# Kernel tuning notes

Measured on AMD Instinct MI355X. Metric: run time of the kernel, lower is better.

Reference implementation:

```python
import jax, jax.numpy as jnp
import numpy as np

K = 3
STRIDE = 1
PAD = 1


def conv2d(x, w, b):
    # standard NCHW conv, stride 1, pad 1
    out = jax.lax.conv_general_dilated(
        x, w, (STRIDE, STRIDE), [(PAD, PAD), (PAD, PAD)],
        dimension_numbers=("NCHW", "OIHW", "NCHW"))
    return out + b[None, :, None, None]


def deform_conv2d(x, offset, mask, weight):
    # torchvision.ops.deform_conv2d semantics (offset_groups=1):
    # offset: [B, 2*K*K, Ho, Wo] laid out as (k, (y, x)) per kernel tap k (row-major)
    # mask:   [B, K*K, Ho, Wo]
    B, C, H, W = x.shape
    KK = K * K
    Ho, Wo = offset.shape[2:]
    off = offset.reshape(B, KK, 2, Ho, Wo)

    # base sampling positions: p = out*stride - pad + kernel_tap + offset
    tap_y = jnp.repeat(jnp.arange(K, dtype=x.dtype), K)  # [KK]
    tap_x = jnp.tile(jnp.arange(K, dtype=x.dtype), K)    # [KK]
    grid_y = jnp.arange(Ho, dtype=x.dtype) * STRIDE - PAD
    grid_x = jnp.arange(Wo, dtype=x.dtype) * STRIDE - PAD
    py = grid_y[None, None, :, None] + tap_y[None, :, None, None] + off[:, :, 0]  # [B,KK,Ho,Wo]
    px = grid_x[None, None, None, :] + tap_x[None, :, None, None] + off[:, :, 1]

    y0 = jnp.floor(py)
    x0 = jnp.floor(px)
    wy1 = py - y0  # fractional parts
    wx1 = px - x0

    xf = x.reshape(B, C, H * W)

    def gather(yi, xi):
        # zero-padding semantics: out-of-bounds corners contribute 0
        valid = (yi >= 0) & (yi <= H - 1) & (xi >= 0) & (xi <= W - 1)
        idx = (jnp.clip(yi, 0, H - 1) * W + jnp.clip(xi, 0, W - 1)).astype(jnp.int32)
        v = jnp.take_along_axis(xf, idx.reshape(B, 1, KK * Ho * Wo), axis=2)
        v = v.reshape(B, C, KK, Ho, Wo)
        return v * valid[:, None].astype(x.dtype)

    e = lambda a: a[:, None]  # [B,KK,Ho,Wo] -> [B,1,KK,Ho,Wo]
    sampled = (gather(y0, x0) * e((1 - wy1) * (1 - wx1))
               + gather(y0, x0 + 1) * e((1 - wy1) * wx1)
               + gather(y0 + 1, x0) * e(wy1 * (1 - wx1))
               + gather(y0 + 1, x0 + 1) * e(wy1 * wx1))
    sampled = sampled * mask[:, None]  # modulated, [B,C,KK,Ho,Wo]

    Cout = weight.shape[0]
    out = jnp.einsum("bckhw,ock->bohw", sampled, weight.reshape(Cout, C, KK))
    return out


def setup_inputs() -> dict:
    key = jax.random.key(0)
    ks = jax.random.split(key, 5)
    B, Cin, Cout, H, W = 4, 128, 256, 64, 64
    x = jax.random.normal(ks[0], (B, Cin, H, W), jnp.float32)
    # offset/modulator convs are zero-init in the module; use small random weights
    # so the deformable sampling path is actually exercised
    offset_w = jax.random.normal(ks[1], (2 * K * K, Cin, K, K), jnp.float32) * 0.02
    offset_b = jax.random.normal(ks[2], (2 * K * K,), jnp.float32) * 0.1
    mod_w = jax.random.normal(ks[3], (K * K, Cin, K, K), jnp.float32) * 0.02
    mod_b = jnp.zeros((K * K,), jnp.float32)
    weight = jax.random.normal(ks[4], (Cout, Cin, K, K), jnp.float32) * (1.0 / np.sqrt(Cin * K * K))
    return {"x": x, "offset_w": offset_w, "offset_b": offset_b,
            "mod_w": mod_w, "mod_b": mod_b, "weight": weight}


def reference(x, offset_w, offset_b, mod_w, mod_b, weight):
    H, W = x.shape[2], x.shape[3]
    max_offset = max(H, W) / 4.0
    offset = jnp.clip(conv2d(x, offset_w, offset_b), -max_offset, max_offset)
    mask = 2.0 * jax.nn.sigmoid(conv2d(x, mod_w, mod_b))
    return deform_conv2d(x, offset, mask, weight)
```

## Files before the change

kernel.cpp:

```cpp
#include <hip/hip_runtime.h>
#include <math.h>

#define CIN   128
#define COUT  256
#define HH    64
#define WW    64
#define BB    4
#define KK    9
#define CK    (CIN*KK)

typedef unsigned short u16;
typedef unsigned int   u32;
using f32x4  = __attribute__((ext_vector_type(4))) float;
using s16x8  = __attribute__((ext_vector_type(8))) short;

__device__ __forceinline__ u16 f2bf(float f) {
    union { float f; u32 u; } v; v.f = f;
    u32 u = v.u;
    u += 0x7FFFu + ((u >> 16) & 1u);
    return (u16)(u >> 16);
}
__device__ __forceinline__ float bfel(s16x8 v, int j) {
    union { u32 u; float f; } c; c.u = ((u32)(u16)v[j]) << 16; return c.f;
}
__device__ __forceinline__ u32 asu(float f) {
    union { float f; u32 u; } v; v.f = f; return v.u;
}

__global__ __launch_bounds__(256)
void prep_all(const float* __restrict__ x, const float* __restrict__ w,
              const float* __restrict__ ow, const float* __restrict__ mw,
              u16* __restrict__ xt, u16* __restrict__ wfrag,
              u16* __restrict__ wofsf) {
    __shared__ u16 T[64][130];
    int blk = blockIdx.x;
    int tid = threadIdx.x;

    if (blk < 256) {
        int b = blk >> 6, y = blk & 63;
        int lane = tid & 63, cw = tid >> 6;
        for (int c = cw; c < 128; c += 4)
            T[lane][c] = f2bf(x[((b * 128 + c) * 64 + y) * 64 + lane]);
        __syncthreads();
        int c = tid & 127;
        for (int p = tid >> 7; p < 64; p += 2)
            xt[((b * 64 + y) * 64 + p) * 128 + c] = T[p][c];
    } else if (blk < 256 + 1152) {
        int i = (blk - 256) * 256 + tid;
        int j    = i & 7;
        int lane = (i >> 3) & 63;
        int ks4  = (i >> 9) & 3;
        int t    = (i >> 11) & 1;
        int wv   = (i >> 12) & 7;
        int tap  = i >> 15;
        int co = (wv * 2 + t) * 16 + (lane & 15);
        int k  = tap * 128 + ks4 * 32 + (lane >> 4) * 8 + j;
        int c  = k & 127;
        wfrag[i] = f2bf(w[co * CK + c * 9 + tap]);
    } else {
        int i = (blk - 1408) * 256 + tid;
        if (i < 9 * 4096) {
            int j    = i & 7;
            int lane = (i >> 3) & 63;
            int ks4  = (i >> 9) & 3;
            int t    = (i >> 11) & 1;
            int tap  = i >> 12;
            int co = t * 16 + (lane & 15);
            int k  = tap * 128 + ks4 * 32 + (lane >> 4) * 8 + j;
            int c  = k & 127;
            float v = 0.f;
            if (co < 18)      v = ow[co * CK + c * 9 + tap];
            else if (co < 27) v = mw[(co - 18) * CK + c * 9 + tap];
            wofsf[i] = f2bf(v);
        }
    }
}

__global__ __launch_bounds__(512, 4)
void dcn_fused(const u16* __restrict__ xt, const u16* __restrict__ wofsf,
               const float* __restrict__ ob, const float* __restrict__ mb,
               const u16* __restrict__ wfrag, float* __restrict__ out) {
    int blkid = blockIdx.x;
    int xcd = blkid & 7, idx = blkid >> 3;
    int b   = xcd >> 1;
    int ho  = ((xcd & 1) << 5) + (idx >> 1);
    int wo0 = (idx & 1) << 5;
    int tid = threadIdx.x;

    __shared__ __align__(16) u16 Sm[4][32][136];
    __shared__ float s_om[27][32];
    __shared__ int   s_idx[32][KK][4];
    __shared__ float s_wgt[32][KK][4];

    int wv   = tid >> 6, lane = tid & 63;
    int quad = lane >> 4, l16 = lane & 15;
    int gpx  = wv * 4 + (lane >> 4);
    int oct  = lane & 15;

    const u16* xtb = xt + (size_t)b * 4096 * 128;
    const s16x8 vzero = {0,0,0,0,0,0,0,0};

    int pa_ph = wv & 1;
    f32x4 aco[2];
    aco[0] = (f32x4)(0.f); aco[1] = (f32x4)(0.f);

    s16x8 sA[2][2];
    auto pa_gather = [&](int tap, int sp, int ti) {
        int kx = tap % 3;
        int y  = ho - 1 + tap / 3;
        bool yok = (unsigned)y < HH;
        int col = wo0 + gpx + kx - 1;
        bool ok = yok && ((unsigned)col < WW);
        int yc = yok ? y : 0;
        int cc = ((unsigned)col < WW) ? col : 0;
        s16x8 v = *(const s16x8*)(xtb + (size_t)(yc * 64 + cc) * 128 + oct * 8);
        sA[sp][ti] = ok ? v : vzero;
    };

    auto pa_mfma_tap = [&](int tap, int slot) {
        const u16* wc = wofsf + tap * 4096 + lane * 8;
#pragma unroll
        for (int ks4 = 0; ks4 < 4; ++ks4) {
            s16x8 bfrag = *(const s16x8*)(&Sm[slot][pa_ph * 16 + l16][ks4 * 32 + quad * 8]);
#pragma unroll
            for (int t = 0; t < 2; ++t) {
                s16x8 afrag = *(const s16x8*)(wc + (t * 4 + ks4) * 512);
                aco[t] = __builtin_amdgcn_mfma_f32_16x16x32_bf16(afrag, bfrag, aco[t], 0, 0, 0);
            }
        }
    };

    pa_gather(0, 0, 0);
    pa_gather(1, 0, 1);
#pragma unroll
    for (int p = 0; p < 4; ++p) {
        int sp = p & 1;
        *(s16x8*)(&Sm[2 * sp    ][gpx][oct * 8]) = sA[sp][0];
        *(s16x8*)(&Sm[2 * sp + 1][gpx][oct * 8]) = sA[sp][1];
        __syncthreads();
        if (p < 3) { pa_gather(2 * p + 2, sp ^ 1, 0); pa_gather(2 * p + 3, sp ^ 1, 1); }
        else       { pa_gather(8,         sp ^ 1, 0); }
        if (wv < 2) {
            pa_mfma_tap(2 * p,     2 * sp);
            pa_mfma_tap(2 * p + 1, 2 * sp + 1);
        }
    }
    *(s16x8*)(&Sm[0][gpx][oct * 8]) = sA[0][0];
    __syncthreads();
    if (wv < 2) pa_mfma_tap(8, 0);

    if (wv < 2) {
#pragma unroll
        for (int t = 0; t < 2; ++t) {
#pragma unroll
            for (int r = 0; r < 4; ++r) {
                int co = t * 16 + quad * 4 + r;
                if (co < 27) {
                    float v = aco[t][r];
                    if (co < 18) {
                        v += ob[co];
                        v = fminf(fmaxf(v, -16.f), 16.f);
                    } else {
                        v += mb[co - 18];
                        v = 2.f / (1.f + expf(-v));
                    }
                    s_om[co][pa_ph * 16 + l16] = v;
                }
            }
        }
    }
    __syncthreads();

    if (tid < 32 * KK) {
        int p = tid / KK, k = tid - (tid / KK) * KK;
        int wo = wo0 + p;
        float offy = s_om[2 * k][p];
        float offx = s_om[2 * k + 1][p];
        float mval = s_om[18 + k][p];

        float py = (float)(ho - 1 + k / 3) + offy;
        float px = (float)(wo - 1 + k % 3) + offx;
        float y0f = floorf(py), x0f = floorf(px);
        float wy1 = py - y0f,  wx1 = px - x0f;
        float wy0 = 1.f - wy1, wx0 = 1.f - wx1;
        int iy0 = (int)y0f, ix0 = (int)x0f;
        int iy1 = iy0 + 1,  ix1 = ix0 + 1;
        bool vy0 = (iy0 >= 0) && (iy0 < HH);
        bool vy1 = (iy1 >= 0) && (iy1 < HH);
        bool vx0 = (ix0 >= 0) && (ix0 < WW);
        bool vx1 = (ix1 >= 0) && (ix1 < WW);
        int cy0 = min(max(iy0, 0), HH - 1), cy1 = min(max(iy1, 0), HH - 1);
        int cx0 = min(max(ix0, 0), WW - 1), cx1 = min(max(ix1, 0), WW - 1);
        s_idx[p][k][0] = (cy0 * WW + cx0) * 128;
        s_idx[p][k][1] = (cy0 * WW + cx1) * 128;
        s_idx[p][k][2] = (cy1 * WW + cx0) * 128;
        s_idx[p][k][3] = (cy1 * WW + cx1) * 128;
        s_wgt[p][k][0] = (vy0 && vx0) ? mval * wy0 * wx0 : 0.f;
        s_wgt[p][k][1] = (vy0 && vx1) ? mval * wy0 * wx1 : 0.f;
        s_wgt[p][k][2] = (vy1 && vx0) ? mval * wy1 * wx0 : 0.f;
        s_wgt[p][k][3] = (vy1 && vx1) ? mval * wy1 * wx1 : 0.f;
    }
    __syncthreads();

    f32x4 acc[2][2];
#pragma unroll
    for (int t = 0; t < 2; ++t) { acc[t][0] = (f32x4)(0.f); acc[t][1] = (f32x4)(0.f); }

    s16x8 crs[2][2][4];
    float gs[2][2][4];
    auto gatherB = [&](int tap, int sp, int ti) {
        int i0 = s_idx[gpx][tap][0], i1 = s_idx[gpx][tap][1];
        int i2 = s_idx[gpx][tap][2], i3 = s_idx[gpx][tap][3];
        gs[sp][ti][0] = s_wgt[gpx][tap][0]; gs[sp][ti][1] = s_wgt[gpx][tap][1];
        gs[sp][ti][2] = s_wgt[gpx][tap][2]; gs[sp][ti][3] = s_wgt[gpx][tap][3];
        int co8 = oct * 8;
        crs[sp][ti][0] = *(const s16x8*)(xtb + i0 + co8);
        crs[sp][ti][1] = *(const s16x8*)(xtb + i1 + co8);
        crs[sp][ti][2] = *(const s16x8*)(xtb + i2 + co8);
        crs[sp][ti][3] = *(const s16x8*)(xtb + i3 + co8);
    };

    auto blend_store = [&](int sp, int ti, int slot) {
        float g0 = gs[sp][ti][0], g1 = gs[sp][ti][1];
        float g2 = gs[sp][ti][2], g3 = gs[sp][ti][3];
        float o[8];
#pragma unroll
        for (int j = 0; j < 8; ++j)
            o[j] = g0 * bfel(crs[sp][ti][0], j) + g1 * bfel(crs[sp][ti][1], j)
                 + g2 * bfel(crs[sp][ti][2], j) + g3 * bfel(crs[sp][ti][3], j);
        uint4 pkv;
        pkv.x = (asu(o[1]) & 0xFFFF0000u) | (asu(o[0]) >> 16);
        pkv.y = (asu(o[3]) & 0xFFFF0000u) | (asu(o[2]) >> 16);
        pkv.z = (asu(o[5]) & 0xFFFF0000u) | (asu(o[4]) >> 16);
        pkv.w = (asu(o[7]) & 0xFFFF0000u) | (asu(o[6]) >> 16);
        *(uint4*)(&Sm[slot][gpx][oct * 8]) = pkv;
    };

    auto pb_mfma_tap = [&](int tap, int slot) {
        const u16* wc = wfrag + (tap * 8 + wv) * 4096 + lane * 8;
        s16x8 af[8];
#pragma unroll
        for (int t = 0; t < 2; ++t)
#pragma unroll
            for (int ks4 = 0; ks4 < 4; ++ks4)
                af[t * 4 + ks4] = *(const s16x8*)(wc + (t * 4 + ks4) * 512);
#pragma unroll
        for (int ks4 = 0; ks4 < 4; ++ks4) {
            s16x8 bf0 = *(const s16x8*)(&Sm[slot][l16][ks4 * 32 + quad * 8]);
            s16x8 bf1 = *(const s16x8*)(&Sm[slot][16 + l16][ks4 * 32 + quad * 8]);
#pragma unroll
            for (int t = 0; t < 2; ++t) {
                acc[t][0] = __builtin_amdgcn_mfma_f32_16x16x32_bf16(af[t * 4 + ks4], bf0, acc[t][0], 0, 0, 0);
                acc[t][1] = __builtin_amdgcn_mfma_f32_16x16x32_bf16(af[t * 4 + ks4], bf1, acc[t][1], 0, 0, 0);
            }
        }
    };

    gatherB(0, 0, 0);
    gatherB(1, 0, 1);
#pragma unroll
    for (int p = 0; p < 4; ++p) {
        int sp = p & 1;
        blend_store(sp, 0, 2 * sp);
        blend_store(sp, 1, 2 * sp + 1);
        __syncthreads();
        if (p < 3) { gatherB(2 * p + 2, sp ^ 1, 0); gatherB(2 * p + 3, sp ^ 1, 1); }
        else       { gatherB(8,         sp ^ 1, 0); }
        pb_mfma_tap(2 * p,     2 * sp);
        pb_mfma_tap(2 * p + 1, 2 * sp + 1);
    }
    blend_store(0, 0, 0);
    __syncthreads();
    pb_mfma_tap(8, 0);

#pragma unroll
    for (int t = 0; t < 2; ++t) {
        int cobase = (wv * 2 + t) * 16 + quad * 4;
#pragma unroll
        for (int ph = 0; ph < 2; ++ph) {
#pragma unroll
            for (int r = 0; r < 4; ++r) {
                int co = cobase + r;
                out[((b * COUT + co) * HH + ho) * WW + wo0 + ph * 16 + l16] = acc[t][ph][r];
            }
        }
    }
}

extern "C" void kernel_launch(void* const* d_in, const int* in_sizes, int n_in,
                              void* d_out, int out_size, void* d_ws, size_t ws_size,
                              hipStream_t stream) {
    const float* x  = (const float*)d_in[0];
    const float* ow = (const float*)d_in[1];
    const float* ob = (const float*)d_in[2];
    const float* mw = (const float*)d_in[3];
    const float* mb = (const float*)d_in[4];
    const float* wt = (const float*)d_in[5];

    char* ws = (char*)d_ws;
    u16* wfrag = (u16*)ws;  ws += (size_t)COUT * CK * 2;
    u16* wofsf = (u16*)ws;  ws += (size_t)32 * CK * 2;
    u16* xt    = (u16*)ws;
    float* out = (float*)d_out;

    prep_all<<<1552, 256, 0, stream>>>(x, wt, ow, mw, xt, wfrag, wofsf);

    dcn_fused<<<BB * HH * 2, 512, 0, stream>>>(xt, wofsf, ob, mb, wfrag, out);
}
```

Measured before the change: 104.1 us.

## Compute offset/mask conv with direct global loads across four waves, no LDS staging

The offset/modulator 3x3 conv prologue stops staging input pixels through shared memory in a double-buffered loop with barriers. Four waves now each compute one 16-channel by 16-pixel tile and load B fragments straight from global memory (the channels-last bf16 input) into the MFMA. Before, two waves did all the MFMAs. This removes the per-tap __syncthreads and LDS round-trips and spreads the MFMA work over more waves. The cost is redundant global loads, since each pixel row is read by two waves, and no software prefetch to hide load latency.

Measured after the change: 105.4 us. No clear change (+1.2%).

```diff
diff --git a/kernel.cpp b/kernel.cpp
--- a/kernel.cpp
+++ b/kernel.cpp
@@ -100,72 +100,41 @@
     const u16* xtb = xt + (size_t)b * 4096 * 128;
     const s16x8 vzero = {0,0,0,0,0,0,0,0};
 
-    int pa_ph = wv & 1;
-    f32x4 aco[2];
-    aco[0] = (f32x4)(0.f); aco[1] = (f32x4)(0.f);
-
-    s16x8 sA[2][2];
-    auto pa_gather = [&](int tap, int sp, int ti) {
-        int kx = tap % 3;
-        int y  = ho - 1 + tap / 3;
-        bool yok = (unsigned)y < HH;
-        int col = wo0 + gpx + kx - 1;
-        bool ok = yok && ((unsigned)col < WW);
-        int yc = yok ? y : 0;
-        int cc = ((unsigned)col < WW) ? col : 0;
-        s16x8 v = *(const s16x8*)(xtb + (size_t)(yc * 64 + cc) * 128 + oct * 8);
-        sA[sp][ti] = ok ? v : vzero;
-    };
-
-    auto pa_mfma_tap = [&](int tap, int slot) {
-        const u16* wc = wofsf + tap * 4096 + lane * 8;
-#pragma unroll
-        for (int ks4 = 0; ks4 < 4; ++ks4) {
-            s16x8 bfrag = *(const s16x8*)(&Sm[slot][pa_ph * 16 + l16][ks4 * 32 + quad * 8]);
-#pragma unroll
-            for (int t = 0; t < 2; ++t) {
-                s16x8 afrag = *(const s16x8*)(wc + (t * 4 + ks4) * 512);
-                aco[t] = __builtin_amdgcn_mfma_f32_16x16x32_bf16(afrag, bfrag, aco[t], 0, 0, 0);
-            }
-        }
-    };
-
-    pa_gather(0, 0, 0);
-    pa_gather(1, 0, 1);
-#pragma unroll
-    for (int p = 0; p < 4; ++p) {
-        int sp = p & 1;
-        *(s16x8*)(&Sm[2 * sp    ][gpx][oct * 8]) = sA[sp][0];
-        *(s16x8*)(&Sm[2 * sp + 1][gpx][oct * 8]) = sA[sp][1];
-        __syncthreads();
-        if (p < 3) { pa_gather(2 * p + 2, sp ^ 1, 0); pa_gather(2 * p + 3, sp ^ 1, 1); }
-        else       { pa_gather(8,         sp ^ 1, 0); }
-        if (wv < 2) {
-            pa_mfma_tap(2 * p,     2 * sp);
-            pa_mfma_tap(2 * p + 1, 2 * sp + 1);
-        }
-    }
-    *(s16x8*)(&Sm[0][gpx][oct * 8]) = sA[0][0];
-    __syncthreads();
-    if (wv < 2) pa_mfma_tap(8, 0);
-
-    if (wv < 2) {
-#pragma unroll
-        for (int t = 0; t < 2; ++t) {
-#pragma unroll
-            for (int r = 0; r < 4; ++r) {
-                int co = t * 16 + quad * 4 + r;
-                if (co < 27) {
-                    float v = aco[t][r];
-                    if (co < 18) {
-                        v += ob[co];
-                        v = fminf(fmaxf(v, -16.f), 16.f);
-                    } else {
-                        v += mb[co - 18];
-                        v = 2.f / (1.f + expf(-v));
-                    }
-                    s_om[co][pa_ph * 16 + l16] = v;
+    if (wv < 4) {
+        int t  = wv & 1;
+        int ph = wv >> 1;
+        f32x4 aco = (f32x4)(0.f);
+        int col0 = wo0 + ph * 16 + l16 - 1;
+#pragma unroll
+        for (int tap = 0; tap < KK; ++tap) {
+            int y   = ho - 1 + tap / 3;
+            int col = col0 + tap % 3;
+            bool ok = ((unsigned)y < HH) && ((unsigned)col < WW);
+            int yc = ((unsigned)y < HH) ? y : 0;
+            int cc = ((unsigned)col < WW) ? col : 0;
+            const u16* src = xtb + (size_t)(yc * 64 + cc) * 128 + quad * 8;
+            const u16* wc  = wofsf + tap * 4096 + t * 2048 + lane * 8;
+#pragma unroll
+            for (int ks4 = 0; ks4 < 4; ++ks4) {
+                s16x8 bf = *(const s16x8*)(src + ks4 * 32);
+                bf = ok ? bf : vzero;
+                s16x8 af = *(const s16x8*)(wc + ks4 * 512);
+                aco = __builtin_amdgcn_mfma_f32_16x16x32_bf16(af, bf, aco, 0, 0, 0);
+            }
+        }
+#pragma unroll
+        for (int r = 0; r < 4; ++r) {
+            int co = t * 16 + quad * 4 + r;
+            if (co < 27) {
+                float v = aco[r];
+                if (co < 18) {
+                    v += ob[co];
+                    v = fminf(fmaxf(v, -16.f), 16.f);
+                } else {
+                    v += mb[co - 18];
+                    v = 2.f / (1.f + expf(-v));
                 }
+                s_om[co][ph * 16 + l16] = v;
             }
         }
     }
```
